# Kernel optimization log

Measured on AMD Instinct MI355X. Metric: run time of the kernel, lower is better.

The kernel has to match this reference:

```python
import jax, jax.numpy as jnp
import numpy as np

N = 100000          # number of agents
H = 1024            # hidden_dim
GS = 8              # grid_size
NB = 4.0            # neighborhood radius (L-inf)


def setup_inputs() -> dict:
    key = jax.random.key(0)
    k1, k2, k3, k4 = jax.random.split(key, 4)
    h_states = jax.random.normal(k1, (N, H), dtype=jnp.float32)
    positions = jax.random.uniform(k2, (N, 2), dtype=jnp.float32) * 20.0 - 10.0  # in [-10,10]
    W = jax.random.normal(k3, (H, H), dtype=jnp.float32) * (1.0 / np.sqrt(H))  # embed.weight
    b = jax.random.normal(k4, (H,), dtype=jnp.float32) * 0.01                  # embed.bias
    return {"h_states": h_states, "positions": positions, "idx": 5, "W": W, "b": b}


def reference(h_states, positions, idx, W, b):
    n = h_states.shape[0]
    diff = positions - positions[idx]                      # (N,2) relative positions
    mask = (jnp.max(jnp.abs(diff), axis=1) <= NB) & (jnp.arange(n) != idx)
    # torch does float clamp to [0, GS-1] then int() truncation (== floor since >=0)
    val = jnp.clip((diff / NB + 1.0) * 0.5 * GS, 0.0, GS - 1)
    g = jnp.floor(val).astype(jnp.int32)                   # (N,2) -> (gx, gy)
    cell = g[:, 1] * GS + g[:, 0]                          # (N,)
    mf = mask.astype(h_states.dtype)
    grid = jax.ops.segment_sum(h_states * mf[:, None], cell, num_segments=GS * GS)  # (GS*GS, H)
    counts = jax.ops.segment_sum(mf, cell, num_segments=GS * GS)                    # (GS*GS,)
    counts = jnp.maximum(counts, 1.0)
    pooled = (grid / counts[:, None]).sum(axis=0)          # (H,)
    return pooled @ W.T + b
```

## Files before the change

### kernel.cpp

```cpp
#include <hip/hip_runtime.h>

#define HDIM 1024
#define GS 8
#define NBR 4.0f
#define HIST_APB 4096
#define NSP 32

__device__ __forceinline__ int agent_cell(float px, float py, float p0x, float p0y,
                                          int i, int idx, bool* m)
{
    float dx = px - p0x, dy = py - p0y;
    *m = (fmaxf(fabsf(dx), fabsf(dy)) <= NBR) && (i != idx);
    float vx = fminf(fmaxf((dx / NBR + 1.0f) * 0.5f * (float)GS, 0.0f), (float)(GS - 1));
    float vy = fminf(fmaxf((dy / NBR + 1.0f) * 0.5f * (float)GS, 0.0f), (float)(GS - 1));
    return (int)vy * GS + (int)vx;
}

__launch_bounds__(256)
__global__ void k_hist(const float2* __restrict__ pos, const int* __restrict__ idxp,
                       int n, int* __restrict__ hist_g, float* __restrict__ partials)
{
    __shared__ int hist[64];
    int tid = threadIdx.x;
    if (tid < 64) hist[tid] = 0;
    __syncthreads();

    int idx = idxp[0];
    float2 p0 = pos[idx];

    int a0 = blockIdx.x * HIST_APB + tid * 16;

    if (a0 + 16 <= n) {
        const float4* pp = (const float4*)pos;
#pragma unroll
        for (int k = 0; k < 8; ++k) {
            float4 q = pp[(a0 >> 1) + k];
            bool m0, m1;
            int c0 = agent_cell(q.x, q.y, p0.x, p0.y, a0 + k * 2,     idx, &m0);
            int c1 = agent_cell(q.z, q.w, p0.x, p0.y, a0 + k * 2 + 1, idx, &m1);
            if (m0) atomicAdd(&hist[c0], 1);
            if (m1) atomicAdd(&hist[c1], 1);
        }
    } else {
        for (int k = 0; k < 16; ++k) {
            int i = a0 + k;
            if (i < n) {
                float2 p = pos[i];
                bool m;
                int c = agent_cell(p.x, p.y, p0.x, p0.y, i, idx, &m);
                if (m) atomicAdd(&hist[c], 1);
            }
        }
    }
    __syncthreads();
    if (tid < 64) hist_g[blockIdx.x * 64 + tid] = hist[tid];

    for (int r = blockIdx.x; r < NSP; r += gridDim.x)
        ((float4*)(partials + (size_t)r * HDIM))[tid] = make_float4(0.f, 0.f, 0.f, 0.f);
}

__launch_bounds__(256)
__global__ void k_reduce(const float* __restrict__ h, const float2* __restrict__ pos,
                         const int* __restrict__ idxp, const int* __restrict__ hist_g,
                         int nbh, int n, float* __restrict__ partials)
{
    __shared__ int   cnt[64];
    __shared__ float inv[65];
    __shared__ int   llist[264];
    __shared__ int   wcnt[4];

    int tid  = threadIdx.x;
    int wave = tid >> 6, lane = tid & 63;

    if (tid < 64) cnt[tid] = 0;
    __syncthreads();

    {
        int s = 0;
        for (int b = wave; b < nbh; b += 4)
            s += hist_g[b * 64 + lane];
        atomicAdd(&cnt[lane], s);
    }

    int idx = idxp[0];
    float2 p0 = pos[idx];
    int i = blockIdx.x * 256 + tid;
    bool m = false;
    int cv = 0;
    if (i < n) {
        float2 p = pos[i];
        cv = agent_cell(p.x, p.y, p0.x, p0.y, i, idx, &m);
    }

    __syncthreads();
    if (tid < 64) inv[tid] = 1.0f / (float)(cnt[tid] > 1 ? cnt[tid] : 1);
    if (tid == 64) inv[64] = 0.0f;

    unsigned long long bal = __ballot(m);
    if (lane == 0) wcnt[wave] = __popcll(bal);
    int ppos = __popcll(bal & ((1ull << lane) - 1ull));
    __syncthreads();

    int off = 0;
    for (int w2 = 0; w2 < wave; ++w2) off += wcnt[w2];
    int lc = wcnt[0] + wcnt[1] + wcnt[2] + wcnt[3];
    int lcp = (lc + 7) & ~7;
    if (m) llist[off + ppos] = (i << 8) | cv;
    if (tid >= lc && tid < lcp) llist[tid] = 64;
    __syncthreads();

    if (lcp == 0) return;

    float4 acc = make_float4(0.f, 0.f, 0.f, 0.f);
    for (int g = 0; g < lcp; g += 8) {
        int e[8];
        float4 v[8];
#pragma unroll
        for (int k = 0; k < 8; ++k) e[k] = llist[g + k];
#pragma unroll
        for (int k = 0; k < 8; ++k)
            v[k] = ((const float4*)(h + (size_t)(e[k] >> 8) * HDIM))[tid];
#pragma unroll
        for (int k = 0; k < 8; ++k) {
            float w = inv[e[k] & 255];
            acc.x += w * v[k].x; acc.y += w * v[k].y;
            acc.z += w * v[k].z; acc.w += w * v[k].w;
        }
    }

    float* pr = partials + (size_t)(blockIdx.x & (NSP - 1)) * HDIM + tid * 4;
    atomicAdd(&pr[0], acc.x);
    atomicAdd(&pr[1], acc.y);
    atomicAdd(&pr[2], acc.z);
    atomicAdd(&pr[3], acc.w);
}

__launch_bounds__(256)
__global__ void k_matvec(const float* __restrict__ W, const float* __restrict__ bvec,
                         const float* __restrict__ partials, float* __restrict__ out)
{
    __shared__ float pooled_s[HDIM];
    int tid  = threadIdx.x;
    int wave = tid >> 6, lane = tid & 63;

    float4 s = make_float4(0.f, 0.f, 0.f, 0.f);
#pragma unroll 8
    for (int r = 0; r < NSP; ++r) {
        float4 v = ((const float4*)(partials + (size_t)r * HDIM))[tid];
        s.x += v.x; s.y += v.y; s.z += v.z; s.w += v.w;
    }
    ((float4*)pooled_s)[tid] = s;
    __syncthreads();

    int j = blockIdx.x * 4 + wave;
    const float4* Wr = (const float4*)(W + (size_t)j * HDIM);
    float d = 0.f;
#pragma unroll
    for (int q = 0; q < 4; ++q) {
        float4 wv = Wr[lane + q * 64];
        float4 pv = ((const float4*)pooled_s)[lane + q * 64];
        d += wv.x * pv.x + wv.y * pv.y + wv.z * pv.z + wv.w * pv.w;
    }

    for (int offr = 32; offr > 0; offr >>= 1)
        d += __shfl_down(d, offr, 64);

    if (lane == 0)
        out[j] = d + bvec[j];
}

extern "C" void kernel_launch(void* const* d_in, const int* in_sizes, int n_in,
                              void* d_out, int out_size, void* d_ws, size_t ws_size,
                              hipStream_t stream) {
    const float*  h    = (const float*)d_in[0];
    const float2* pos  = (const float2*)d_in[1];
    const int*    idxp = (const int*)d_in[2];
    const float*  W    = (const float*)d_in[3];
    const float*  bvec = (const float*)d_in[4];
    float* out = (float*)d_out;

    int n = in_sizes[0] / HDIM;

    int nbh = (n + HIST_APB - 1) / HIST_APB;
    int nbr = (n + 255) / 256;

    char* ws = (char*)d_ws;
    int*   hist_g   = (int*)ws;
    size_t off1     = ((size_t)nbh * 64 * 4 + 255) & ~(size_t)255;
    float* partials = (float*)(ws + off1);

    k_hist  <<<nbh, 256, 0, stream>>>(pos, idxp, n, hist_g, partials);
    k_reduce<<<nbr, 256, 0, stream>>>(h, pos, idxp, hist_g, nbh, n, partials);
    k_matvec<<<HDIM / 4, 256, 0, stream>>>(W, bvec, partials, out);
}
```

Measured before the change: 30.36 us.

## Hoist per-cell weight computation into separate kernel and deepen gather unroll

Adds a single-block kernel that sums the per-block histograms once and writes the 65 inverse-count weights to global memory. Each reduce block then loads these weights instead of re-summing all histogram blocks itself. The gather loop is also widened from 8 to 16 rows in flight, padding the list to a multiple of 16, to raise memory-level parallelism. The cost is an extra kernel launch on the serial path and higher register pressure in the reduce kernel.

```diff
diff --git a/kernel.cpp b/kernel.cpp
--- a/kernel.cpp
+++ b/kernel.cpp
@@ -29,15 +29,14 @@
     float2 p0 = pos[idx];
 
     int a0 = blockIdx.x * HIST_APB + tid * 16;
-
     if (a0 + 16 <= n) {
         const float4* pp = (const float4*)pos;
 #pragma unroll
         for (int k = 0; k < 8; ++k) {
             float4 q = pp[(a0 >> 1) + k];
             bool m0, m1;
-            int c0 = agent_cell(q.x, q.y, p0.x, p0.y, a0 + k * 2,     idx, &m0);
-            int c1 = agent_cell(q.z, q.w, p0.x, p0.y, a0 + k * 2 + 1, idx, &m1);
+            int c0 = agent_cell(q.x, q.y, p0.x, p0.y, a0 + 2 * k,     idx, &m0);
+            int c1 = agent_cell(q.z, q.w, p0.x, p0.y, a0 + 2 * k + 1, idx, &m1);
             if (m0) atomicAdd(&hist[c0], 1);
             if (m1) atomicAdd(&hist[c1], 1);
         }
@@ -60,27 +59,38 @@
 }
 
 __launch_bounds__(256)
+__global__ void k_weights(const int* __restrict__ hist_g, int nbh,
+                          float* __restrict__ inv_g)
+{
+    __shared__ int cnt2[64];
+    int tid = threadIdx.x;
+    if (tid < 64) cnt2[tid] = 0;
+    __syncthreads();
+
+    {
+        int c = tid & 63, s = 0;
+        for (int b = tid >> 6; b < nbh; b += 4)
+            s += hist_g[b * 64 + c];
+        atomicAdd(&cnt2[c], s);
+    }
+    __syncthreads();
+    if (tid < 64) inv_g[tid] = 1.0f / (float)(cnt2[tid] > 1 ? cnt2[tid] : 1);
+    if (tid == 64) inv_g[64] = 0.0f;
+}
+
+__launch_bounds__(256)
 __global__ void k_reduce(const float* __restrict__ h, const float2* __restrict__ pos,
-                         const int* __restrict__ idxp, const int* __restrict__ hist_g,
-                         int nbh, int n, float* __restrict__ partials)
-{
-    __shared__ int   cnt[64];
+                         const int* __restrict__ idxp, const float* __restrict__ inv_g,
+                         int n, float* __restrict__ partials)
+{
     __shared__ float inv[65];
-    __shared__ int   llist[264];
+    __shared__ int   llist[272];
     __shared__ int   wcnt[4];
 
     int tid  = threadIdx.x;
     int wave = tid >> 6, lane = tid & 63;
 
-    if (tid < 64) cnt[tid] = 0;
-    __syncthreads();
-
-    {
-        int s = 0;
-        for (int b = wave; b < nbh; b += 4)
-            s += hist_g[b * 64 + lane];
-        atomicAdd(&cnt[lane], s);
-    }
+    if (tid < 65) inv[tid] = inv_g[tid];
 
     int idx = idxp[0];
     float2 p0 = pos[idx];
@@ -92,10 +102,6 @@
         cv = agent_cell(p.x, p.y, p0.x, p0.y, i, idx, &m);
     }
 
-    __syncthreads();
-    if (tid < 64) inv[tid] = 1.0f / (float)(cnt[tid] > 1 ? cnt[tid] : 1);
-    if (tid == 64) inv[64] = 0.0f;
-
     unsigned long long bal = __ballot(m);
     if (lane == 0) wcnt[wave] = __popcll(bal);
     int ppos = __popcll(bal & ((1ull << lane) - 1ull));
@@ -104,7 +110,7 @@
     int off = 0;
     for (int w2 = 0; w2 < wave; ++w2) off += wcnt[w2];
     int lc = wcnt[0] + wcnt[1] + wcnt[2] + wcnt[3];
-    int lcp = (lc + 7) & ~7;
+    int lcp = (lc + 15) & ~15;
     if (m) llist[off + ppos] = (i << 8) | cv;
     if (tid >= lc && tid < lcp) llist[tid] = 64;
     __syncthreads();
@@ -112,16 +118,16 @@
     if (lcp == 0) return;
 
     float4 acc = make_float4(0.f, 0.f, 0.f, 0.f);
-    for (int g = 0; g < lcp; g += 8) {
-        int e[8];
-        float4 v[8];
-#pragma unroll
-        for (int k = 0; k < 8; ++k) e[k] = llist[g + k];
-#pragma unroll
-        for (int k = 0; k < 8; ++k)
+    for (int g = 0; g < lcp; g += 16) {
+        int e[16];
+        float4 v[16];
+#pragma unroll
+        for (int k = 0; k < 16; ++k) e[k] = llist[g + k];
+#pragma unroll
+        for (int k = 0; k < 16; ++k)
             v[k] = ((const float4*)(h + (size_t)(e[k] >> 8) * HDIM))[tid];
 #pragma unroll
-        for (int k = 0; k < 8; ++k) {
+        for (int k = 0; k < 16; ++k) {
             float w = inv[e[k] & 255];
             acc.x += w * v[k].x; acc.y += w * v[k].y;
             acc.z += w * v[k].z; acc.w += w * v[k].w;
@@ -186,10 +192,13 @@
 
     char* ws = (char*)d_ws;
     int*   hist_g   = (int*)ws;
-    size_t off1     = ((size_t)nbh * 64 * 4 + 255) & ~(size_t)255;
-    float* partials = (float*)(ws + off1);
-
-    k_hist  <<<nbh, 256, 0, stream>>>(pos, idxp, n, hist_g, partials);
-    k_reduce<<<nbr, 256, 0, stream>>>(h, pos, idxp, hist_g, nbh, n, partials);
-    k_matvec<<<HDIM / 4, 256, 0, stream>>>(W, bvec, partials, out);
-}
+    size_t off1 = ((size_t)nbh * 64 * 4 + 255) & ~(size_t)255;
+    float* inv_g    = (float*)(ws + off1);
+    size_t off2 = off1 + 512;
+    float* partials = (float*)(ws + off2);
+
+    k_hist   <<<nbh, 256, 0, stream>>>(pos, idxp, n, hist_g, partials);
+    k_weights<<<1,   256, 0, stream>>>(hist_g, nbh, inv_g);
+    k_reduce <<<nbr, 256, 0, stream>>>(h, pos, idxp, inv_g, n, partials);
+    k_matvec <<<HDIM / 4, 256, 0, stream>>>(W, bvec, partials, out);
+}
```

Result: slower. 32.72 us (+7.8%).
